# Performance work log

Hardware: AMD Instinct MI355X
Metric: run time of the kernel (lower is better)

Reference implementation:

```python
import jax, jax.numpy as jnp
import numpy as np

B, NQ, NK, QS, KS, H, VD = 16, 64, 512, 256, 256, 256, 256


def setup_inputs() -> dict:
    key = jax.random.key(0)
    k1, k2, k3, k4, k5, k6, k7 = jax.random.split(key, 7)
    return {
        "queries": jax.random.normal(k1, (B, NQ, QS), dtype=jnp.float32),
        "keys": jax.random.normal(k2, (B, NK, KS), dtype=jnp.float32),
        "values": jax.random.normal(k3, (B, NK, VD), dtype=jnp.float32),
        "valid_lens": jax.random.randint(k4, (B,), 1, NK + 1, dtype=jnp.int32),
        # learned params (nn.Linear with bias=False): W_q [QS,H], W_k [KS,H], w_v [H]
        "W_q": jax.random.normal(k5, (QS, H), dtype=jnp.float32) / np.sqrt(QS),
        "W_k": jax.random.normal(k6, (KS, H), dtype=jnp.float32) / np.sqrt(KS),
        "w_v": jax.random.normal(k7, (H,), dtype=jnp.float32) / np.sqrt(H),
    }


def reference(queries, keys, values, valid_lens, W_q, W_k, w_v):
    # project: q [B,nq,H], k [B,nk,H]
    q = jnp.einsum("bqd,dh->bqh", queries, W_q)
    k = jnp.einsum("bkd,dh->bkh", keys, W_k)
    # broadcast-add -> tanh -> score reduction via w_v: [B,nq,nk]
    features = jnp.tanh(q[:, :, None, :] + k[:, None, :, :])  # [B,nq,nk,H]
    scores = jnp.einsum("bqkh,h->bqk", features, w_v)
    # masked softmax over keys (positions >= valid_len masked out)
    mask = jnp.arange(scores.shape[-1])[None, None, :] < valid_lens[:, None, None]
    scores = jnp.where(mask, scores, -1e6)
    attn = jax.nn.softmax(scores, axis=-1)
    # weighted sum of values (dropout p=0 / eval mode => identity)
    return jnp.einsum("bqk,bkv->bqv", attn, values)
```

## Files before the change

### kernel.cpp

```cpp
#include <hip/hip_runtime.h>
#include <hip/hip_bf16.h>

#define BB 16
#define NQ 64
#define NK 512
#define HD 256

typedef __attribute__((ext_vector_type(8))) short short8;
typedef __attribute__((ext_vector_type(4))) float f32x4;

__device__ __forceinline__ ushort bf16_rne(float v) {
    unsigned u = __float_as_uint(v);
    return (ushort)((u + 0x7FFFu + ((u >> 16) & 1u)) >> 16);
}
__device__ __forceinline__ float bf16_to_f(ushort h) {
    return __uint_as_float(((unsigned)h) << 16);
}

__global__ __launch_bounds__(256) void convert_split(
    const float* __restrict__ q, const float* __restrict__ k,
    const float* __restrict__ wq, const float* __restrict__ wk,
    ushort* __restrict__ qh, ushort* __restrict__ ql,
    ushort* __restrict__ kh, ushort* __restrict__ kl,
    ushort* __restrict__ wqh, ushort* __restrict__ wql,
    ushort* __restrict__ wkh, ushort* __restrict__ wkl)
{
    const int idx = blockIdx.x * 256 + threadIdx.x;
    if (blockIdx.x < 2304) {
        int e = idx * 4;
        const float* src; ushort *dh, *dl; int off;
        if (e < 1024 * 256) { src = q; dh = qh; dl = ql; off = e; }
        else { src = k; dh = kh; dl = kl; off = e - 1024 * 256; }
        float4 v = *(const float4*)&src[off];
        float fv[4] = {v.x, v.y, v.z, v.w};
        ushort hh[4], ll[4];
        #pragma unroll
        for (int c = 0; c < 4; ++c) {
            hh[c] = bf16_rne(fv[c]);
            ll[c] = bf16_rne(fv[c] - bf16_to_f(hh[c]));
        }
        *(ushort4*)&dh[off] = make_ushort4(hh[0], hh[1], hh[2], hh[3]);
        *(ushort4*)&dl[off] = make_ushort4(ll[0], ll[1], ll[2], ll[3]);
    } else {
        int widx = idx - 2304 * 256;
        const float* W; ushort *wh, *wl;
        if (widx < 16384) { W = wq; wh = wqh; wl = wql; }
        else { W = wk; wh = wkh; wl = wkl; widx -= 16384; }
        int n  = widx >> 6;
        int k4 = (widx & 63) * 4;
        ushort hh[4], ll[4];
        #pragma unroll
        for (int c = 0; c < 4; ++c) {
            float v = W[(k4 + c) * 256 + n];
            hh[c] = bf16_rne(v);
            ll[c] = bf16_rne(v - bf16_to_f(hh[c]));
        }
        *(ushort4*)&wh[n * 256 + k4] = make_ushort4(hh[0], hh[1], hh[2], hh[3]);
        *(ushort4*)&wl[n * 256 + k4] = make_ushort4(ll[0], ll[1], ll[2], ll[3]);
    }
}

__global__ __launch_bounds__(256, 2) void proj_mfma2(
    const ushort* __restrict__ qh, const ushort* __restrict__ ql,
    const ushort* __restrict__ kh, const ushort* __restrict__ kl,
    const ushort* __restrict__ wqh, const ushort* __restrict__ wql,
    const ushort* __restrict__ wkh, const ushort* __restrict__ wkl,
    float* __restrict__ qp, float* __restrict__ kp, float scale)
{
    __shared__ ushort AsH[128 * 64], AsL[128 * 64];
    __shared__ ushort BsH[64 * 64],  BsL[64 * 64];

    const ushort *Ah, *Al, *Bh, *Bl; float* C; int rows0;
    if (blockIdx.x < 8) { Ah = qh; Al = ql; Bh = wqh; Bl = wql; C = qp; rows0 = blockIdx.x * 128; }
    else                { Ah = kh; Al = kl; Bh = wkh; Bl = wkl; C = kp; rows0 = (blockIdx.x - 8) * 128; }
    const int cols0 = blockIdx.y * 64;

    const int t = threadIdx.x, lane = t & 63, wave = t >> 6;
    const int quad = lane >> 4, l15 = lane & 15;
    const int lr = lane >> 3;
    const int cg = (lane & 7) ^ lr;
    const int swz0 = quad ^ (l15 & 7);
    const int swz1 = (quad + 4) ^ (l15 & 7);

    f32x4 acc[2][4];
    #pragma unroll
    for (int i = 0; i < 2; ++i)
        #pragma unroll
        for (int j = 0; j < 4; ++j)
            acc[i][j] = (f32x4){0.f, 0.f, 0.f, 0.f};

    short8 rAh[4], rAl[4], rBh[2], rBl[2];
    #pragma unroll
    for (int i = 0; i < 4; ++i) {
        size_t g = (size_t)(rows0 + (wave * 4 + i) * 8 + lr) * 256 + cg * 8;
        rAh[i] = *(const short8*)&Ah[g];
        rAl[i] = *(const short8*)&Al[g];
    }
    #pragma unroll
    for (int j = 0; j < 2; ++j) {
        size_t g = (size_t)(cols0 + (wave * 2 + j) * 8 + lr) * 256 + cg * 8;
        rBh[j] = *(const short8*)&Bh[g];
        rBl[j] = *(const short8*)&Bl[g];
    }

    for (int k0 = 0; k0 < 256; k0 += 64) {
        __syncthreads();
        #pragma unroll
        for (int i = 0; i < 4; ++i) {
            int ci = (wave * 4 + i) * 64 + lane;
            *(short8*)&AsH[ci * 8] = rAh[i];
            *(short8*)&AsL[ci * 8] = rAl[i];
        }
        #pragma unroll
        for (int j = 0; j < 2; ++j) {
            int ci = (wave * 2 + j) * 64 + lane;
            *(short8*)&BsH[ci * 8] = rBh[j];
            *(short8*)&BsL[ci * 8] = rBl[j];
        }
        __syncthreads();

        if (k0 + 64 < 256) {
            #pragma unroll
            for (int i = 0; i < 4; ++i) {
                size_t g = (size_t)(rows0 + (wave * 4 + i) * 8 + lr) * 256 + k0 + 64 + cg * 8;
                rAh[i] = *(const short8*)&Ah[g];
                rAl[i] = *(const short8*)&Al[g];
            }
            #pragma unroll
            for (int j = 0; j < 2; ++j) {
                size_t g = (size_t)(cols0 + (wave * 2 + j) * 8 + lr) * 256 + k0 + 64 + cg * 8;
                rBh[j] = *(const short8*)&Bh[g];
                rBl[j] = *(const short8*)&Bl[g];
            }
        }

        #pragma unroll
        for (int ks = 0; ks < 2; ++ks) {
            const int s = ks ? swz1 : swz0;
            short8 aH[2], aL[2], bH[4], bL[4];
            #pragma unroll
            for (int ms = 0; ms < 2; ++ms) {
                int r = wave * 32 + ms * 16 + l15;
                aH[ms] = *(const short8*)&AsH[r * 64 + s * 8];
                aL[ms] = *(const short8*)&AsL[r * 64 + s * 8];
            }
            #pragma unroll
            for (int ns = 0; ns < 4; ++ns) {
                int n = ns * 16 + l15;
                bH[ns] = *(const short8*)&BsH[n * 64 + s * 8];
                bL[ns] = *(const short8*)&BsL[n * 64 + s * 8];
            }
            #pragma unroll
            for (int ms = 0; ms < 2; ++ms)
                #pragma unroll
                for (int ns = 0; ns < 4; ++ns)
                    acc[ms][ns] = __builtin_amdgcn_mfma_f32_16x16x32_bf16(aH[ms], bH[ns], acc[ms][ns], 0, 0, 0);
            #pragma unroll
            for (int ms = 0; ms < 2; ++ms)
                #pragma unroll
                for (int ns = 0; ns < 4; ++ns)
                    acc[ms][ns] = __builtin_amdgcn_mfma_f32_16x16x32_bf16(aL[ms], bH[ns], acc[ms][ns], 0, 0, 0);
            #pragma unroll
            for (int ms = 0; ms < 2; ++ms)
                #pragma unroll
                for (int ns = 0; ns < 4; ++ns)
                    acc[ms][ns] = __builtin_amdgcn_mfma_f32_16x16x32_bf16(aH[ms], bL[ns], acc[ms][ns], 0, 0, 0);
        }
    }

    #pragma unroll
    for (int ms = 0; ms < 2; ++ms) {
        int rbase = rows0 + wave * 32 + ms * 16 + quad * 4;
        #pragma unroll
        for (int ns = 0; ns < 4; ++ns) {
            int col = cols0 + ns * 16 + l15;
            #pragma unroll
            for (int r = 0; r < 4; ++r)
                C[(size_t)(rbase + r) * 256 + col] = acc[ms][ns][r] * scale;
        }
    }
}

__global__ __launch_bounds__(256) void score_kernel(
    const float* __restrict__ qp,
    const float* __restrict__ kp,
    const int*   __restrict__ vlens,
    const float* __restrict__ w_v,
    float* __restrict__ S)
{
    __shared__ float qs[32][260];
    __shared__ float ks[16][260];
    __shared__ float wv[HD];

    const int b     = blockIdx.x;
    const int chunk = blockIdx.y;
    const int qhalf = blockIdx.z;
    const int vl    = vlens[b];
    if (chunk * 16 >= vl) return;

    const int t    = threadIdx.x;
    const int lane = t & 63;
    const int wave = t >> 6;

    const float* qsrc = qp + ((size_t)b * NQ + qhalf * 32) * HD;
    #pragma unroll
    for (int i = 0; i < 8; ++i) {
        int idx = i * 256 + t;
        int row = idx >> 6, c4 = (idx & 63) * 4;
        *(float4*)&qs[row][c4] = *(const float4*)&qsrc[(size_t)row * HD + c4];
    }
    const float* ksrc = kp + ((size_t)b * NK + chunk * 16) * HD;
    #pragma unroll
    for (int i = 0; i < 4; ++i) {
        int idx = i * 256 + t;
        int row = idx >> 6, c4 = (idx & 63) * 4;
        *(float4*)&ks[row][c4] = *(const float4*)&ksrc[(size_t)row * HD + c4];
    }
    if (t < 64) *(float4*)&wv[t * 4] = *(const float4*)&w_v[t * 4];
    __syncthreads();

    float Wsum;
    {
        float ws = wv[lane] + wv[lane + 64] + wv[lane + 128] + wv[lane + 192];
        #pragma unroll
        for (int off = 32; off; off >>= 1) ws += __shfl_xor(ws, off);
        Wsum = ws;
    }

    const int qloc = wave * 8 + (lane >> 3);
    const int n0   = (lane & 7) * 2;

    const float* qrow = &qs[qloc][0];
    const float* k0   = &ks[n0][0];
    const float* k1   = &ks[n0 + 1][0];

    float s0 = 0.f, s1 = 0.f;
    #pragma unroll 8
    for (int h4 = 0; h4 < 64; ++h4) {
        float4 q4 = *(const float4*)&qrow[h4 * 4];
        float4 w4 = *(const float4*)&wv[h4 * 4];
        float4 ka = *(const float4*)&k0[h4 * 4];
        float4 kb = *(const float4*)&k1[h4 * 4];
        float qv[4] = {q4.x, q4.y, q4.z, q4.w};
        float wv4[4] = {w4.x, w4.y, w4.z, w4.w};
        float kav[4] = {ka.x, ka.y, ka.z, ka.w};
        float kbv[4] = {kb.x, kb.y, kb.z, kb.w};
        #pragma unroll
        for (int c = 0; c < 4; ++c) {
            float r0 = __builtin_amdgcn_rcpf(__builtin_amdgcn_exp2f(qv[c] + kav[c]) + 1.f);
            float r1 = __builtin_amdgcn_rcpf(__builtin_amdgcn_exp2f(qv[c] + kbv[c]) + 1.f);
            s0 = fmaf(wv4[c], r0, s0);
            s1 = fmaf(wv4[c], r1, s1);
        }
    }
    float2 o;
    o.x = fmaf(-2.f, s0, Wsum);
    o.y = fmaf(-2.f, s1, Wsum);
    const int qg = qhalf * 32 + qloc;
    *(float2*)&S[((size_t)b * NQ + qg) * NK + chunk * 16 + n0] = o;
}

__global__ __launch_bounds__(256, 2) void softmax_pv(
    const float* __restrict__ S,
    const float* __restrict__ values,
    const int*   __restrict__ vlens,
    float* __restrict__ out)
{
    __shared__ float sc[2][NK];
    __shared__ float part[4][2][HD];
    __shared__ float redm[4], reds[4], invs[2];

    const int b     = blockIdx.x & 15;
    const int qpair = blockIdx.x >> 4;
    const int qi0   = qpair * 2;
    const int t     = threadIdx.x;
    const int lane  = t & 63;
    const int wave  = t >> 6;
    const int vl    = vlens[b];
    const int vla   = (vl + 15) & ~15;
    const size_t row0 = (size_t)b * NQ + qi0;

    const float* S0 = &S[row0 * NK];
    const float* S1 = &S[(row0 + 1) * NK];
    for (int n = t; n < vla; n += 256) { sc[0][n] = S0[n]; sc[1][n] = S1[n]; }
    __syncthreads();

    {
        const int qq  = wave >> 1;
        const int sub = wave & 1;
        float m = -1e30f;
        for (int n = sub * 64 + lane; n < vl; n += 128) m = fmaxf(m, sc[qq][n]);
        #pragma unroll
        for (int off = 32; off; off >>= 1) m = fmaxf(m, __shfl_xor(m, off));
        if (lane == 0) redm[wave] = m;
        __syncthreads();
        m = fmaxf(redm[qq * 2], redm[qq * 2 + 1]);

        float ssum = 0.f;
        const float L2E = 1.4426950408889634f;
        for (int n = sub * 64 + lane; n < vl; n += 128) {
            float p = __builtin_amdgcn_exp2f((sc[qq][n] - m) * L2E);
            sc[qq][n] = p;
            ssum += p;
        }
        #pragma unroll
        for (int off = 32; off; off >>= 1) ssum += __shfl_xor(ssum, off);
        if (lane == 0) reds[wave] = ssum;
        if (vl + t < vla) { sc[0][vl + t] = 0.f; sc[1][vl + t] = 0.f; }
        __syncthreads();
        if (t == 0)  invs[0] = __builtin_amdgcn_rcpf(reds[0] + reds[1]);
        if (t == 64) invs[1] = __builtin_amdgcn_rcpf(reds[2] + reds[3]);
    }
    __syncthreads();

    float4 acc0 = {0.f, 0.f, 0.f, 0.f};
    float4 acc1 = {0.f, 0.f, 0.f, 0.f};
    const float* vbase = values + (size_t)b * NK * HD;
    for (int nb = wave * 4; nb < vla; nb += 16) {
        float4 v[4]; float pa[4], pb[4];
        #pragma unroll
        for (int u = 0; u < 4; ++u) {
            v[u]  = *(const float4*)&vbase[(size_t)(nb + u) * HD + lane * 4];
            pa[u] = sc[0][nb + u];
            pb[u] = sc[1][nb + u];
        }
        #pragma unroll
        for (int u = 0; u < 4; ++u) {
            acc0.x = fmaf(pa[u], v[u].x, acc0.x);
            acc0.y = fmaf(pa[u], v[u].y, acc0.y);
            acc0.z = fmaf(pa[u], v[u].z, acc0.z);
            acc0.w = fmaf(pa[u], v[u].w, acc0.w);
            acc1.x = fmaf(pb[u], v[u].x, acc1.x);
            acc1.y = fmaf(pb[u], v[u].y, acc1.y);
            acc1.z = fmaf(pb[u], v[u].z, acc1.z);
            acc1.w = fmaf(pb[u], v[u].w, acc1.w);
        }
    }
    *(float4*)&part[wave][0][lane * 4] = acc0;
    *(float4*)&part[wave][1][lane * 4] = acc1;
    __syncthreads();

    if (wave < 2) {
        float4 p0 = *(const float4*)&part[0][wave][lane * 4];
        float4 p1 = *(const float4*)&part[1][wave][lane * 4];
        float4 p2 = *(const float4*)&part[2][wave][lane * 4];
        float4 p3 = *(const float4*)&part[3][wave][lane * 4];
        const float inv = invs[wave];
        float4 o;
        o.x = ((p0.x + p1.x) + (p2.x + p3.x)) * inv;
        o.y = ((p0.y + p1.y) + (p2.y + p3.y)) * inv;
        o.z = ((p0.z + p1.z) + (p2.z + p3.z)) * inv;
        o.w = ((p0.w + p1.w) + (p2.w + p3.w)) * inv;
        *(float4*)&out[(row0 + wave) * HD + lane * 4] = o;
    }
}

extern "C" void kernel_launch(void* const* d_in, const int* in_sizes, int n_in,
                              void* d_out, int out_size, void* d_ws, size_t ws_size,
                              hipStream_t stream) {
    const float* queries = (const float*)d_in[0];
    const float* keys    = (const float*)d_in[1];
    const float* values  = (const float*)d_in[2];
    const int*   vlens   = (const int*)d_in[3];
    const float* W_q     = (const float*)d_in[4];
    const float* W_k     = (const float*)d_in[5];
    const float* w_v     = (const float*)d_in[6];
    float* out = (float*)d_out;

    float*  kp  = (float*)d_ws;
    float*  qp  = kp + (size_t)BB * NK * HD;
    float*  S   = qp + (size_t)BB * NQ * HD;
    ushort* qh  = (ushort*)(S + (size_t)BB * NQ * NK);
    ushort* ql  = qh  + 1024 * 256;
    ushort* kh  = ql  + 1024 * 256;
    ushort* kl  = kh  + 8192 * 256;
    ushort* wqh = kl  + 8192 * 256;
    ushort* wql = wqh + 65536;
    ushort* wkh = wql + 65536;
    ushort* wkl = wkh + 65536;

    const float SC = 2.885390081777927f;

    convert_split<<<dim3(2432), 256, 0, stream>>>(queries, keys, W_q, W_k,
                                                  qh, ql, kh, kl,
                                                  wqh, wql, wkh, wkl);
    proj_mfma2<<<dim3(72, 4), 256, 0, stream>>>(qh, ql, kh, kl,
                                                wqh, wql, wkh, wkl,
                                                qp, kp, SC);
    score_kernel<<<dim3(16, 32, 2), 256, 0, stream>>>(qp, kp, vlens, w_v, S);
    softmax_pv<<<dim3(512), 256, 0, stream>>>(S, values, vlens, out);
}
```

Measured before the change: 127.6 us.

## Fuse score, local softmax and PV into split-K flash-style partials with combine

Replaces the separate score and softmax+PV kernels with a kernel that, per 16-key chunk, computes the additive-attention scores for all 64 queries, takes a local max and exp-sum, and multiplies by the chunk's values to write partial outputs. A second small kernel merges the chunk partials with log-sum-exp rescaling. This removes the full score matrix round trip and the separate values pass. In exchange it writes and rereads a large per-chunk partial-output buffer of 64x256 floats per chunk, and each block now handles all queries with fewer blocks (512 instead of 1024 score blocks), which lowers parallelism.

```diff
diff --git a/kernel.cpp b/kernel.cpp
--- a/kernel.cpp
+++ b/kernel.cpp
@@ -181,40 +181,39 @@
     }
 }
 
-__global__ __launch_bounds__(256) void score_kernel(
+__global__ __launch_bounds__(256) void score_pv_partial(
     const float* __restrict__ qp,
     const float* __restrict__ kp,
+    const float* __restrict__ values,
     const int*   __restrict__ vlens,
     const float* __restrict__ w_v,
-    float* __restrict__ S)
+    float* __restrict__ pO,
+    float* __restrict__ pM,
+    float* __restrict__ pL)
 {
-    __shared__ float qs[32][260];
     __shared__ float ks[16][260];
+    __shared__ float vs_[16][260];
+    __shared__ float qs[16][260];
     __shared__ float wv[HD];
-
-    const int b     = blockIdx.x;
-    const int chunk = blockIdx.y;
-    const int qhalf = blockIdx.z;
+    __shared__ float Ps[64][20];
+    __shared__ float msub[64], lsub[64];
+
+    const int b     = blockIdx.x >> 5;
+    const int chunk = blockIdx.x & 31;
     const int vl    = vlens[b];
     if (chunk * 16 >= vl) return;
 
     const int t    = threadIdx.x;
     const int lane = t & 63;
-    const int wave = t >> 6;
-
-    const float* qsrc = qp + ((size_t)b * NQ + qhalf * 32) * HD;
-    #pragma unroll
-    for (int i = 0; i < 8; ++i) {
-        int idx = i * 256 + t;
-        int row = idx >> 6, c4 = (idx & 63) * 4;
-        *(float4*)&qs[row][c4] = *(const float4*)&qsrc[(size_t)row * HD + c4];
-    }
-    const float* ksrc = kp + ((size_t)b * NK + chunk * 16) * HD;
+
+    const float* kbase = kp + ((size_t)b * NK + chunk * 16) * HD;
+    const float* vbase = values + ((size_t)b * NK + chunk * 16) * HD;
     #pragma unroll
     for (int i = 0; i < 4; ++i) {
         int idx = i * 256 + t;
         int row = idx >> 6, c4 = (idx & 63) * 4;
-        *(float4*)&ks[row][c4] = *(const float4*)&ksrc[(size_t)row * HD + c4];
+        *(float4*)&ks[row][c4]  = *(const float4*)&kbase[(size_t)row * HD + c4];
+        *(float4*)&vs_[row][c4] = *(const float4*)&vbase[(size_t)row * HD + c4];
     }
     if (t < 64) *(float4*)&wv[t * 4] = *(const float4*)&w_v[t * 4];
     __syncthreads();
@@ -227,132 +226,127 @@
         Wsum = ws;
     }
 
-    const int qloc = wave * 8 + (lane >> 3);
-    const int n0   = (lane & 7) * 2;
-
-    const float* qrow = &qs[qloc][0];
-    const float* k0   = &ks[n0][0];
-    const float* k1   = &ks[n0 + 1][0];
-
-    float s0 = 0.f, s1 = 0.f;
-    #pragma unroll 8
-    for (int h4 = 0; h4 < 64; ++h4) {
-        float4 q4 = *(const float4*)&qrow[h4 * 4];
-        float4 w4 = *(const float4*)&wv[h4 * 4];
-        float4 ka = *(const float4*)&k0[h4 * 4];
-        float4 kb = *(const float4*)&k1[h4 * 4];
-        float qv[4] = {q4.x, q4.y, q4.z, q4.w};
-        float wv4[4] = {w4.x, w4.y, w4.z, w4.w};
-        float kav[4] = {ka.x, ka.y, ka.z, ka.w};
-        float kbv[4] = {kb.x, kb.y, kb.z, kb.w};
-        #pragma unroll
-        for (int c = 0; c < 4; ++c) {
-            float r0 = __builtin_amdgcn_rcpf(__builtin_amdgcn_exp2f(qv[c] + kav[c]) + 1.f);
-            float r1 = __builtin_amdgcn_rcpf(__builtin_amdgcn_exp2f(qv[c] + kbv[c]) + 1.f);
-            s0 = fmaf(wv4[c], r0, s0);
-            s1 = fmaf(wv4[c], r1, s1);
-        }
-    }
-    float2 o;
-    o.x = fmaf(-2.f, s0, Wsum);
-    o.y = fmaf(-2.f, s1, Wsum);
-    const int qg = qhalf * 32 + qloc;
-    *(float2*)&S[((size_t)b * NQ + qg) * NK + chunk * 16 + n0] = o;
-}
-
-__global__ __launch_bounds__(256, 2) void softmax_pv(
-    const float* __restrict__ S,
-    const float* __restrict__ values,
-    const int*   __restrict__ vlens,
+    const int qloc = t >> 4;
+    const int kl   = t & 15;
+    const float L2E = 1.4426950408889634f;
+    const bool masked = (chunk * 16 + kl >= vl);
+
+    for (int g = 0; g < 4; ++g) {
+        const float* qsrc = qp + ((size_t)b * NQ + g * 16) * HD;
+        #pragma unroll
+        for (int i = 0; i < 4; ++i) {
+            int idx = i * 256 + t;
+            int row = idx >> 6, c4 = (idx & 63) * 4;
+            *(float4*)&qs[row][c4] = *(const float4*)&qsrc[(size_t)row * HD + c4];
+        }
+        __syncthreads();
+
+        const float* qrow = &qs[qloc][0];
+        const float* krow = &ks[kl][0];
+        float s0 = 0.f, s1 = 0.f;
+        #pragma unroll 4
+        for (int h8 = 0; h8 < 32; ++h8) {
+            float4 qa = *(const float4*)&qrow[h8 * 8];
+            float4 qb = *(const float4*)&qrow[h8 * 8 + 4];
+            float4 ka = *(const float4*)&krow[h8 * 8];
+            float4 kb = *(const float4*)&krow[h8 * 8 + 4];
+            float4 wa = *(const float4*)&wv[h8 * 8];
+            float4 wb = *(const float4*)&wv[h8 * 8 + 4];
+            s0 = fmaf(wa.x, __builtin_amdgcn_rcpf(__builtin_amdgcn_exp2f(qa.x + ka.x) + 1.f), s0);
+            s0 = fmaf(wa.y, __builtin_amdgcn_rcpf(__builtin_amdgcn_exp2f(qa.y + ka.y) + 1.f), s0);
+            s0 = fmaf(wa.z, __builtin_amdgcn_rcpf(__builtin_amdgcn_exp2f(qa.z + ka.z) + 1.f), s0);
+            s0 = fmaf(wa.w, __builtin_amdgcn_rcpf(__builtin_amdgcn_exp2f(qa.w + ka.w) + 1.f), s0);
+            s1 = fmaf(wb.x, __builtin_amdgcn_rcpf(__builtin_amdgcn_exp2f(qb.x + kb.x) + 1.f), s1);
+            s1 = fmaf(wb.y, __builtin_amdgcn_rcpf(__builtin_amdgcn_exp2f(qb.y + kb.y) + 1.f), s1);
+            s1 = fmaf(wb.z, __builtin_amdgcn_rcpf(__builtin_amdgcn_exp2f(qb.z + kb.z) + 1.f), s1);
+            s1 = fmaf(wb.w, __builtin_amdgcn_rcpf(__builtin_amdgcn_exp2f(qb.w + kb.w) + 1.f), s1);
+        }
+        float s = fmaf(-2.f, s0 + s1, Wsum);
+        if (masked) s = -1e6f;
+
+        float m = s;
+        m = fmaxf(m, __shfl_xor(m, 8));
+        m = fmaxf(m, __shfl_xor(m, 4));
+        m = fmaxf(m, __shfl_xor(m, 2));
+        m = fmaxf(m, __shfl_xor(m, 1));
+        float e = __builtin_amdgcn_exp2f((s - m) * L2E);
+        float l = e;
+        l += __shfl_xor(l, 8);
+        l += __shfl_xor(l, 4);
+        l += __shfl_xor(l, 2);
+        l += __shfl_xor(l, 1);
+        Ps[g * 16 + qloc][kl] = e;
+        if (kl == 0) { msub[g * 16 + qloc] = m; lsub[g * 16 + qloc] = l; }
+        __syncthreads();
+    }
+
+    const int qg = t >> 2;
+    const int c  = (t & 3) * 4;
+    f32x4 acc[16];
+    #pragma unroll
+    for (int r = 0; r < 16; ++r) acc[r] = (f32x4){0.f, 0.f, 0.f, 0.f};
+
+    #pragma unroll
+    for (int k = 0; k < 16; ++k) {
+        float p = Ps[qg][k];
+        #pragma unroll
+        for (int r = 0; r < 16; ++r) {
+            float4 v = *(const float4*)&vs_[k][c + r * 16];
+            acc[r][0] = fmaf(p, v.x, acc[r][0]);
+            acc[r][1] = fmaf(p, v.y, acc[r][1]);
+            acc[r][2] = fmaf(p, v.z, acc[r][2]);
+            acc[r][3] = fmaf(p, v.w, acc[r][3]);
+        }
+    }
+    float* obase = pO + (((size_t)(b * 32 + chunk)) * 64 + qg) * 256;
+    #pragma unroll
+    for (int r = 0; r < 16; ++r)
+        *(f32x4*)&obase[c + r * 16] = acc[r];
+    if ((t & 3) == 0) {
+        pM[(size_t)(b * 32 + chunk) * 64 + qg] = msub[qg];
+        pL[(size_t)(b * 32 + chunk) * 64 + qg] = lsub[qg];
+    }
+}
+
+__global__ __launch_bounds__(64) void combine_pv(
+    const float* __restrict__ pO, const float* __restrict__ pM,
+    const float* __restrict__ pL, const int* __restrict__ vlens,
     float* __restrict__ out)
 {
-    __shared__ float sc[2][NK];
-    __shared__ float part[4][2][HD];
-    __shared__ float redm[4], reds[4], invs[2];
-
-    const int b     = blockIdx.x & 15;
-    const int qpair = blockIdx.x >> 4;
-    const int qi0   = qpair * 2;
-    const int t     = threadIdx.x;
-    const int lane  = t & 63;
-    const int wave  = t >> 6;
-    const int vl    = vlens[b];
-    const int vla   = (vl + 15) & ~15;
-    const size_t row0 = (size_t)b * NQ + qi0;
-
-    const float* S0 = &S[row0 * NK];
-    const float* S1 = &S[(row0 + 1) * NK];
-    for (int n = t; n < vla; n += 256) { sc[0][n] = S0[n]; sc[1][n] = S1[n]; }
-    __syncthreads();
-
-    {
-        const int qq  = wave >> 1;
-        const int sub = wave & 1;
-        float m = -1e30f;
-        for (int n = sub * 64 + lane; n < vl; n += 128) m = fmaxf(m, sc[qq][n]);
-        #pragma unroll
-        for (int off = 32; off; off >>= 1) m = fmaxf(m, __shfl_xor(m, off));
-        if (lane == 0) redm[wave] = m;
-        __syncthreads();
-        m = fmaxf(redm[qq * 2], redm[qq * 2 + 1]);
-
-        float ssum = 0.f;
-        const float L2E = 1.4426950408889634f;
-        for (int n = sub * 64 + lane; n < vl; n += 128) {
-            float p = __builtin_amdgcn_exp2f((sc[qq][n] - m) * L2E);
-            sc[qq][n] = p;
-            ssum += p;
-        }
-        #pragma unroll
-        for (int off = 32; off; off >>= 1) ssum += __shfl_xor(ssum, off);
-        if (lane == 0) reds[wave] = ssum;
-        if (vl + t < vla) { sc[0][vl + t] = 0.f; sc[1][vl + t] = 0.f; }
-        __syncthreads();
-        if (t == 0)  invs[0] = __builtin_amdgcn_rcpf(reds[0] + reds[1]);
-        if (t == 64) invs[1] = __builtin_amdgcn_rcpf(reds[2] + reds[3]);
-    }
-    __syncthreads();
-
-    float4 acc0 = {0.f, 0.f, 0.f, 0.f};
-    float4 acc1 = {0.f, 0.f, 0.f, 0.f};
-    const float* vbase = values + (size_t)b * NK * HD;
-    for (int nb = wave * 4; nb < vla; nb += 16) {
-        float4 v[4]; float pa[4], pb[4];
-        #pragma unroll
-        for (int u = 0; u < 4; ++u) {
-            v[u]  = *(const float4*)&vbase[(size_t)(nb + u) * HD + lane * 4];
-            pa[u] = sc[0][nb + u];
-            pb[u] = sc[1][nb + u];
-        }
-        #pragma unroll
-        for (int u = 0; u < 4; ++u) {
-            acc0.x = fmaf(pa[u], v[u].x, acc0.x);
-            acc0.y = fmaf(pa[u], v[u].y, acc0.y);
-            acc0.z = fmaf(pa[u], v[u].z, acc0.z);
-            acc0.w = fmaf(pa[u], v[u].w, acc0.w);
-            acc1.x = fmaf(pb[u], v[u].x, acc1.x);
-            acc1.y = fmaf(pb[u], v[u].y, acc1.y);
-            acc1.z = fmaf(pb[u], v[u].z, acc1.z);
-            acc1.w = fmaf(pb[u], v[u].w, acc1.w);
-        }
-    }
-    *(float4*)&part[wave][0][lane * 4] = acc0;
-    *(float4*)&part[wave][1][lane * 4] = acc1;
-    __syncthreads();
-
-    if (wave < 2) {
-        float4 p0 = *(const float4*)&part[0][wave][lane * 4];
-        float4 p1 = *(const float4*)&part[1][wave][lane * 4];
-        float4 p2 = *(const float4*)&part[2][wave][lane * 4];
-        float4 p3 = *(const float4*)&part[3][wave][lane * 4];
-        const float inv = invs[wave];
-        float4 o;
-        o.x = ((p0.x + p1.x) + (p2.x + p3.x)) * inv;
-        o.y = ((p0.y + p1.y) + (p2.y + p3.y)) * inv;
-        o.z = ((p0.z + p1.z) + (p2.z + p3.z)) * inv;
-        o.w = ((p0.w + p1.w) + (p2.w + p3.w)) * inv;
-        *(float4*)&out[(row0 + wave) * HD + lane * 4] = o;
-    }
+    const int b    = blockIdx.x >> 6;
+    const int q    = blockIdx.x & 63;
+    const int lane = threadIdx.x;
+    const int vl   = vlens[b];
+    const int nc   = (vl + 15) >> 4;
+    const float L2E = 1.4426950408889634f;
+
+    float mi = -3e38f, li = 0.f;
+    if (lane < nc) {
+        mi = pM[(size_t)(b * 32 + lane) * 64 + q];
+        li = pL[(size_t)(b * 32 + lane) * 64 + q];
+    }
+    float m = mi;
+    #pragma unroll
+    for (int off = 32; off; off >>= 1) m = fmaxf(m, __shfl_xor(m, off));
+    float we = __builtin_amdgcn_exp2f((mi - m) * L2E);
+    float w  = li * we;
+    float L  = w;
+    #pragma unroll
+    for (int off = 32; off; off >>= 1) L += __shfl_xor(L, off);
+
+    f32x4 acc = (f32x4){0.f, 0.f, 0.f, 0.f};
+    for (int i = 0; i < nc; ++i) {
+        float wi = __shfl(we, i);
+        float4 v = *(const float4*)&pO[(((size_t)(b * 32 + i)) * 64 + q) * 256 + lane * 4];
+        acc[0] = fmaf(wi, v.x, acc[0]);
+        acc[1] = fmaf(wi, v.y, acc[1]);
+        acc[2] = fmaf(wi, v.z, acc[2]);
+        acc[3] = fmaf(wi, v.w, acc[3]);
+    }
+    const float inv = __builtin_amdgcn_rcpf(L);
+    float4 o;
+    o.x = acc[0] * inv; o.y = acc[1] * inv; o.z = acc[2] * inv; o.w = acc[3] * inv;
+    *(float4*)&out[((size_t)(b * 64 + q)) * 256 + lane * 4] = o;
 }
 
 extern "C" void kernel_launch(void* const* d_in, const int* in_sizes, int n_in,
@@ -369,8 +363,10 @@
 
     float*  kp  = (float*)d_ws;
     float*  qp  = kp + (size_t)BB * NK * HD;
-    float*  S   = qp + (size_t)BB * NQ * HD;
-    ushort* qh  = (ushort*)(S + (size_t)BB * NQ * NK);
+    float*  pO  = qp + (size_t)BB * NQ * HD;
+    float*  pM  = pO + (size_t)BB * 32 * 64 * 256;
+    float*  pL  = pM + (size_t)BB * 32 * 64;
+    ushort* qh  = (ushort*)(pL + (size_t)BB * 32 * 64);
     ushort* ql  = qh  + 1024 * 256;
     ushort* kh  = ql  + 1024 * 256;
     ushort* kl  = kh  + 8192 * 256;
@@ -387,6 +383,7 @@
     proj_mfma2<<<dim3(72, 4), 256, 0, stream>>>(qh, ql, kh, kl,
                                                 wqh, wql, wkh, wkl,
                                                 qp, kp, SC);
-    score_kernel<<<dim3(16, 32, 2), 256, 0, stream>>>(qp, kp, vlens, w_v, S);
-    softmax_pv<<<dim3(512), 256, 0, stream>>>(S, values, vlens, out);
-}
+    score_pv_partial<<<dim3(BB * 32), 256, 0, stream>>>(qp, kp, values, vlens,
+                                                        w_v, pO, pM, pL);
+    combine_pv<<<dim3(BB * 64), 64, 0, stream>>>(pO, pM, pL, vlens, out);
+}
```

New measurement: 149.5 us. 1.17x slower.
